# Optimization experiments

Measured on AMD Instinct MI355X. Metric: run time of the kernel, lower is better.

## Reference

```python
import jax, jax.numpy as jnp
import numpy as np

PT, SKIP, CNN_UNITS, RNN_UNITS = 16, 32, 512, 512


def setup_inputs() -> dict:
    key = jax.random.key(0)
    k_x, k_w, k_u = jax.random.split(key, 3)
    B, T, C, H = 128, 512, CNN_UNITS, RNN_UNITS
    # 0.05 scaling keeps the relu GRU recurrence numerically stable
    x = jax.random.normal(k_x, (B, T, C), dtype=jnp.float32)
    W = jax.random.normal(k_w, (C, 3 * H), dtype=jnp.float32) * 0.05
    U = jax.random.normal(k_u, (H, 3 * H), dtype=jnp.float32) * 0.05
    b = jnp.zeros((2, 3 * H), dtype=jnp.float32)  # [input_bias, recurrent_bias] (reset_after=True)
    return {"x": x, "W": W, "U": U, "b": b}


def reference(x, W, U, b):
    B, T, C = x.shape
    H = U.shape[0]
    pt, skip = PT, SKIP
    # pretrans: last pt*skip steps -> (B, pt, skip, C) -> (B, skip, pt, C) -> (B*skip, pt, C)
    s = x[:, -pt * skip:, :]
    s = s.reshape(B, pt, skip, C).transpose(0, 2, 1, 3).reshape(B * skip, pt, C)
    # precompute input projections for all timesteps: (pt, B*skip, 3H)
    xp = jnp.einsum('ntc,ch->tnh', s, W) + b[0]
    b_rec = b[1]

    def step(h, xt):
        rec = h @ U + b_rec                      # (N, 3H)
        xz, xr, xh = jnp.split(xt, 3, axis=-1)
        rz, rr, rh = jnp.split(rec, 3, axis=-1)
        z = jax.nn.sigmoid(xz + rz)
        r = jax.nn.sigmoid(xr + rr)
        hh = jax.nn.relu(xh + r * rh)            # activation='relu'
        h_new = z * h + (1.0 - z) * hh
        return h_new, None

    h0 = jnp.zeros((B * skip, H), dtype=x.dtype)
    h_final, _ = jax.lax.scan(step, h0, xp)
    # posttrans: (B*skip, H) -> (B, skip*H)
    return h_final.reshape(B, skip * H)
```

## Files before the change

kernel.cpp:

```cpp
#include <hip/hip_runtime.h>
#include <cstddef>


typedef unsigned short u16;
typedef __attribute__((ext_vector_type(8))) short short8;
typedef __attribute__((ext_vector_type(8))) u16 u16x8;
typedef __attribute__((ext_vector_type(4))) float floatx4;

#define MFMA16(a, b, c) __builtin_amdgcn_mfma_f32_16x16x32_bf16((a), (b), (c), 0, 0, 0)

__device__ __forceinline__ u16 f32_to_bf16(float f) {
  union { float f; unsigned int u; } c; c.f = f;
  unsigned int u = c.u + 0x7FFFu + ((c.u >> 16) & 1u);
  return (u16)(u >> 16);
}
__device__ __forceinline__ float bf16_to_f32(u16 v) {
  union { unsigned int u; float f; } c; c.u = ((unsigned int)v) << 16;
  return c.f;
}
__device__ __forceinline__ float sigmoidf_(float x) {
  return 1.0f / (1.0f + __expf(-x));
}
__device__ __forceinline__ void gload_lds16(const void* g, void* l) {
  __builtin_amdgcn_global_load_lds(
      (const __attribute__((address_space(1))) unsigned int*)g,
      (__attribute__((address_space(3))) unsigned int*)l, 16, 0, 0);
}

__global__ __launch_bounds__(256)
void pack_x(const float* __restrict__ x, u16* __restrict__ xb) {
  __shared__ u16 sm[64 * 512];
  const int t = blockIdx.x >> 6;
  const int nb = blockIdx.x & 63;
  const int tid = threadIdx.x;
#pragma unroll
  for (int it = 0; it < 16; ++it) {
    int idx = it * 256 + tid;
    int row = idx >> 6, ch = idx & 63;
    int xrow = (nb * 2 + (row >> 5)) * 512 + t * 32 + (row & 31);
    const float* src = x + (size_t)xrow * 512 + ch * 8;
    floatx4 va = *(const floatx4*)src;
    floatx4 vb = *(const floatx4*)(src + 4);
    u16x8 pk;
    pk[0] = f32_to_bf16(va[0]); pk[1] = f32_to_bf16(va[1]);
    pk[2] = f32_to_bf16(va[2]); pk[3] = f32_to_bf16(va[3]);
    pk[4] = f32_to_bf16(vb[0]); pk[5] = f32_to_bf16(vb[1]);
    pk[6] = f32_to_bf16(vb[2]); pk[7] = f32_to_bf16(vb[3]);
    *(u16x8*)&sm[row * 512 + (ch ^ (row & 7)) * 8] = pk;
  }
  __syncthreads();
  u16* dst = xb + (size_t)blockIdx.x * 32768;
#pragma unroll
  for (int it = 0; it < 16; ++it) {
    int idx = it * 256 + tid;
    int row = idx & 63, g = (idx >> 6) & 3, kt = idx >> 8;
    int ch = kt * 4 + g;
    u16x8 vv = *(const u16x8*)&sm[row * 512 + (ch ^ (row & 7)) * 8];
    *(u16x8*)(dst + (size_t)idx * 8) = vv;
  }
}

__global__ void pack_Bt(const float* __restrict__ W, const float* __restrict__ U,
                        u16* __restrict__ Bt) {
  size_t gid = (size_t)blockIdx.x * 256 + threadIdx.x;
  int col = (int)(gid & 63);
  int g   = (int)((gid >> 6) & 3);
  int kt  = (int)((gid >> 8) & 31);
  int cc  = (int)(gid >> 13);
  int c = cc * 64 + col;
  int k0 = kt * 32 + g * 8;
  u16x8 pk;
#pragma unroll
  for (int j = 0; j < 8; ++j) {
    int k = k0 + j;
    float v = (k < 512) ? W[(size_t)k * 1536 + c] : U[(size_t)(k - 512) * 1536 + c];
    pk[j] = f32_to_bf16(v);
  }
  *(u16x8*)(Bt + gid * 8) = pk;
}

__global__ __launch_bounds__(256)
void gru_step(const u16* __restrict__ xb, const u16* __restrict__ Bt,
              const float* __restrict__ bias,
              const u16* __restrict__ h_in, u16* __restrict__ h_out,
              float* __restrict__ out, int t, int first, int last) {
  __shared__ alignas(16) char sm[32768];
  const int tid = threadIdx.x;
  const int idx = blockIdx.x;
  const int nb = ((idx >> 6) << 3) | (idx & 7);
  const int hb = (idx >> 3) & 7;
  const int w = __builtin_amdgcn_readfirstlane(tid >> 6);
  const int lane = tid & 63;
  const int wy = w >> 1, wx = w & 1;
  const int q = lane >> 4, lc = lane & 15;

  const u16* xbB = xb + (size_t)(t * 64 + nb) * 32768;
  const u16* htB = h_in + (size_t)nb * 32768;
  const int cs0 = hb, cs1 = 8 + hb, cs2 = 16 + hb;

  floatx4 acZ[2][2] = {{{0.f,0.f,0.f,0.f},{0.f,0.f,0.f,0.f}},{{0.f,0.f,0.f,0.f},{0.f,0.f,0.f,0.f}}};
  floatx4 acR[2][2] = {{{0.f,0.f,0.f,0.f},{0.f,0.f,0.f,0.f}},{{0.f,0.f,0.f,0.f},{0.f,0.f,0.f,0.f}}};
  floatx4 acX[2][2] = {{{0.f,0.f,0.f,0.f},{0.f,0.f,0.f,0.f}},{{0.f,0.f,0.f,0.f},{0.f,0.f,0.f,0.f}}};
  floatx4 acH[2][2] = {{{0.f,0.f,0.f,0.f},{0.f,0.f,0.f,0.f}},{{0.f,0.f,0.f,0.f},{0.f,0.f,0.f,0.f}}};

  const int ktall = first ? 16 : 32;
  const int wo = w * 1024;

  auto stage = [&](int kt, int bsel) {
    char* lds = sm + bsel * 16384;
    const char* aS = (const char*)((kt < 16) ? (xbB + (size_t)kt * 2048)
                                             : (htB + (size_t)(kt - 16) * 2048));
    gload_lds16(aS + wo + lane * 16, lds + wo);
    gload_lds16((const char*)(Bt + (size_t)(cs0 * 32 + kt) * 2048) + wo + lane * 16,
                lds + 4096 + wo);
    gload_lds16((const char*)(Bt + (size_t)(cs1 * 32 + kt) * 2048) + wo + lane * 16,
                lds + 8192 + wo);
    gload_lds16((const char*)(Bt + (size_t)(cs2 * 32 + kt) * 2048) + wo + lane * 16,
                lds + 12288 + wo);
  };

  auto compute = [&](int bsel, floatx4 (&acT)[2][2]) {
    const char* lds = sm + bsel * 16384;
    short8 a0 = *(const short8*)(lds + (q * 64 + wy * 32 + lc) * 16);
    short8 a1 = *(const short8*)(lds + (q * 64 + wy * 32 + 16 + lc) * 16);
#pragma unroll
    for (int ci = 0; ci < 2; ++ci) {
      int co = (q * 64 + wx * 32 + ci * 16 + lc) * 16;
      short8 bz = *(const short8*)(lds + 4096 + co);
      short8 br = *(const short8*)(lds + 8192 + co);
      short8 bh = *(const short8*)(lds + 12288 + co);
      acZ[0][ci] = MFMA16(a0, bz, acZ[0][ci]);
      acZ[1][ci] = MFMA16(a1, bz, acZ[1][ci]);
      acR[0][ci] = MFMA16(a0, br, acR[0][ci]);
      acR[1][ci] = MFMA16(a1, br, acR[1][ci]);
      acT[0][ci] = MFMA16(a0, bh, acT[0][ci]);
      acT[1][ci] = MFMA16(a1, bh, acT[1][ci]);
    }
  };

  stage(0, 0);
  __syncthreads();
  for (int kt = 0; kt < 16; ++kt) {
    if (kt + 1 < ktall) stage(kt + 1, (kt + 1) & 1);
    compute(kt & 1, acX);
    __syncthreads();
  }
  if (!first) {
    for (int kt = 16; kt < 32; ++kt) {
      if (kt + 1 < 32) stage(kt + 1, (kt + 1) & 1);
      compute(kt & 1, acH);
      __syncthreads();
    }
  }

  const float* b0 = bias;
  const float* b1 = bias + 1536;
  u16* Ct = (u16*)sm;
#pragma unroll
  for (int ci = 0; ci < 2; ++ci) {
    const int hcl = wx * 32 + ci * 16 + lc;
    const int hg = hb * 64 + hcl;
    const float bz = b0[hg] + b1[hg];
    const float br = b0[512 + hg] + b1[512 + hg];
    const float b0h = b0[1024 + hg];
    const float b1h = b1[1024 + hg];
    const int ktg = hg >> 5;
    const int gg = (hg >> 3) & 3;
    const size_t hbase = (((size_t)nb * 16 + ktg) * 4 + gg) * 64;
#pragma unroll
    for (int mi = 0; mi < 2; ++mi) {
#pragma unroll
      for (int reg = 0; reg < 4; ++reg) {
        const int nl = wy * 32 + mi * 16 + q * 4 + reg;
        const int n = nb * 64 + nl;
        float z = sigmoidf_(acZ[mi][ci][reg] + bz);
        float r = sigmoidf_(acR[mi][ci][reg] + br);
        float hh = acX[mi][ci][reg] + b0h + r * (acH[mi][ci][reg] + b1h);
        hh = fmaxf(hh, 0.0f);
        float hp = 0.0f;
        if (!first) hp = bf16_to_f32(h_in[(hbase + nl) * 8 + (hg & 7)]);
        float v = z * hp + (1.0f - z) * hh;
        if (last) out[(size_t)n * 512 + hg] = v;
        else      Ct[nl * 72 + hcl] = f32_to_bf16(v);
      }
    }
  }
  if (!last) {
    __syncthreads();
#pragma unroll
    for (int i = 0; i < 2; ++i) {
      int e = i * 256 + tid;
      int row = e & 63;
      int g = (e >> 6) & 3;
      int ktl = e >> 8;
      u16x8 vv = *(const u16x8*)(Ct + row * 72 + ktl * 32 + g * 8);
      *(u16x8*)(h_out + ((((size_t)nb * 16 + (hb * 2 + ktl)) * 4 + g) * 64 + row) * 8) = vv;
    }
  }
}

extern "C" void kernel_launch(void* const* d_in, const int* in_sizes, int n_in,
                              void* d_out, int out_size, void* d_ws, size_t ws_size,
                              hipStream_t stream) {
  const float* x = (const float*)d_in[0];
  const float* W = (const float*)d_in[1];
  const float* U = (const float*)d_in[2];
  const float* bias = (const float*)d_in[3];
  float* out = (float*)d_out;

  u16* xb = (u16*)d_ws;
  u16* Bt = xb + (size_t)16 * 64 * 32768;
  u16* h0 = Bt + (size_t)1536 * 1024;
  u16* h1 = h0 + (size_t)4096 * 512;

  pack_x<<<1024, 256, 0, stream>>>(x, xb);
  pack_Bt<<<768, 256, 0, stream>>>(W, U, Bt);

  for (int t = 0; t < 16; ++t) {
    const u16* hin = (t & 1) ? h1 : h0;
    u16* hout = (t & 1) ? h0 : h1;
    gru_step<<<512, 256, 0, stream>>>(
        xb, Bt, bias, hin, hout, out, t, (t == 0) ? 1 : 0, (t == 15) ? 1 : 0);
  }
}
```

Before: 522.1 us.

## Deepen GRU step K-loop to 4-stage LDS pipeline with explicit vmcnt waits

Replaces the double-buffered LDS staging in the per-timestep GRU GEMM with a four-buffer ring that keeps three tiles in flight. It uses explicit s_waitcnt vmcnt counts and raw barriers in place of a full __syncthreads after every tile, and raises wave priority around the MFMA compute. The aim is to hide global-to-LDS load latency better. LDS use doubles to 64KB per block, which may cut occupancy. Because the ternary picks the accumulator array by reference, the compute lambda may get harder for the compiler to keep in registers.

```diff
diff --git a/kernel.cpp b/kernel.cpp
--- a/kernel.cpp
+++ b/kernel.cpp
@@ -84,7 +84,7 @@
               const float* __restrict__ bias,
               const u16* __restrict__ h_in, u16* __restrict__ h_out,
               float* __restrict__ out, int t, int first, int last) {
-  __shared__ alignas(16) char sm[32768];
+  __shared__ alignas(16) char sm[65536];
   const int tid = threadIdx.x;
   const int idx = blockIdx.x;
   const int nb = ((idx >> 6) << 3) | (idx & 7);
@@ -139,20 +139,30 @@
   };
 
   stage(0, 0);
+  stage(1, 1);
+  stage(2, 2);
+  int kt = 0;
+  for (; kt < ktall - 2; ++kt) {
+    asm volatile("s_waitcnt vmcnt(8)" ::: "memory");
+    __builtin_amdgcn_s_barrier();
+    if (kt + 3 < ktall) stage(kt + 3, (kt + 3) & 3);
+    __builtin_amdgcn_s_setprio(1);
+    compute(kt & 3, (kt < 16) ? acX : acH);
+    __builtin_amdgcn_s_setprio(0);
+  }
+  asm volatile("s_waitcnt vmcnt(4)" ::: "memory");
+  __builtin_amdgcn_s_barrier();
+  __builtin_amdgcn_s_setprio(1);
+  compute(kt & 3, (kt < 16) ? acX : acH);
+  __builtin_amdgcn_s_setprio(0);
+  ++kt;
+  asm volatile("s_waitcnt vmcnt(0)" ::: "memory");
+  __builtin_amdgcn_s_barrier();
+  __builtin_amdgcn_s_setprio(1);
+  compute(kt & 3, (kt < 16) ? acX : acH);
+  __builtin_amdgcn_s_setprio(0);
+
   __syncthreads();
-  for (int kt = 0; kt < 16; ++kt) {
-    if (kt + 1 < ktall) stage(kt + 1, (kt + 1) & 1);
-    compute(kt & 1, acX);
-    __syncthreads();
-  }
-  if (!first) {
-    for (int kt = 16; kt < 32; ++kt) {
-      if (kt + 1 < 32) stage(kt + 1, (kt + 1) & 1);
-      compute(kt & 1, acH);
-      __syncthreads();
-    }
-  }
-
   const float* b0 = bias;
   const float* b1 = bias + 1536;
   u16* Ct = (u16*)sm;
```

Result: slower. 597.3 us (+14.4%).

## Enlarge GRU step tile to 128 rows with split-K waves and 4-stage pipeline

Applied to the files above, without the earlier changes.

Each gru_step block now covers 128 batch rows instead of 64, using 512 threads, and the grid shrinks from 512 to 256 blocks. Its 8 waves split the K dimension in two, and the halves are summed through LDS before the gate epilogue. Loads use a 4-slot global-to-LDS ring with explicit vmcnt waits, and the MFMA section runs at raised priority. The aim is to reuse the weight tiles across more rows and hide load latency, at the cost of 144KB of dynamic LDS per block, an extra reduction pass, and fewer blocks across the CUs.

```diff
diff --git a/kernel.cpp b/kernel.cpp
--- a/kernel.cpp
+++ b/kernel.cpp
@@ -79,109 +79,195 @@
   *(u16x8*)(Bt + gid * 8) = pk;
 }
 
-__global__ __launch_bounds__(256)
+__global__ __launch_bounds__(512, 2)
 void gru_step(const u16* __restrict__ xb, const u16* __restrict__ Bt,
               const float* __restrict__ bias,
               const u16* __restrict__ h_in, u16* __restrict__ h_out,
               float* __restrict__ out, int t, int first, int last) {
-  __shared__ alignas(16) char sm[32768];
+  extern __shared__ char sm[];
   const int tid = threadIdx.x;
   const int idx = blockIdx.x;
-  const int nb = ((idx >> 6) << 3) | (idx & 7);
-  const int hb = (idx >> 3) & 7;
+  const int nbb = idx & 31;
+  const int hb  = idx >> 5;
   const int w = __builtin_amdgcn_readfirstlane(tid >> 6);
   const int lane = tid & 63;
-  const int wy = w >> 1, wx = w & 1;
+  const int ks = w & 1, wx = (w >> 1) & 1, wy = w >> 2;
   const int q = lane >> 4, lc = lane & 15;
 
-  const u16* xbB = xb + (size_t)(t * 64 + nb) * 32768;
-  const u16* htB = h_in + (size_t)nb * 32768;
-  const int cs0 = hb, cs1 = 8 + hb, cs2 = 16 + hb;
-
-  floatx4 acZ[2][2] = {{{0.f,0.f,0.f,0.f},{0.f,0.f,0.f,0.f}},{{0.f,0.f,0.f,0.f},{0.f,0.f,0.f,0.f}}};
-  floatx4 acR[2][2] = {{{0.f,0.f,0.f,0.f},{0.f,0.f,0.f,0.f}},{{0.f,0.f,0.f,0.f},{0.f,0.f,0.f,0.f}}};
-  floatx4 acX[2][2] = {{{0.f,0.f,0.f,0.f},{0.f,0.f,0.f,0.f}},{{0.f,0.f,0.f,0.f},{0.f,0.f,0.f,0.f}}};
-  floatx4 acH[2][2] = {{{0.f,0.f,0.f,0.f},{0.f,0.f,0.f,0.f}},{{0.f,0.f,0.f,0.f},{0.f,0.f,0.f,0.f}}};
-
-  const int ktall = first ? 16 : 32;
-  const int wo = w * 1024;
-
-  auto stage = [&](int kt, int bsel) {
-    char* lds = sm + bsel * 16384;
-    const char* aS = (const char*)((kt < 16) ? (xbB + (size_t)kt * 2048)
-                                             : (htB + (size_t)(kt - 16) * 2048));
-    gload_lds16(aS + wo + lane * 16, lds + wo);
-    gload_lds16((const char*)(Bt + (size_t)(cs0 * 32 + kt) * 2048) + wo + lane * 16,
-                lds + 4096 + wo);
-    gload_lds16((const char*)(Bt + (size_t)(cs1 * 32 + kt) * 2048) + wo + lane * 16,
-                lds + 8192 + wo);
-    gload_lds16((const char*)(Bt + (size_t)(cs2 * 32 + kt) * 2048) + wo + lane * 16,
-                lds + 12288 + wo);
+  const u16* xbB0 = xb + (size_t)(t * 64 + nbb * 2) * 32768;
+  const u16* htB0 = h_in + (size_t)(nbb * 2) * 32768;
+
+  floatx4 acZ[4][2], acR[4][2], acX[4][2], acH[4][2];
+#pragma unroll
+  for (int f = 0; f < 4; ++f)
+#pragma unroll
+    for (int ci = 0; ci < 2; ++ci) {
+      acZ[f][ci] = (floatx4){0.f, 0.f, 0.f, 0.f};
+      acR[f][ci] = (floatx4){0.f, 0.f, 0.f, 0.f};
+      acX[f][ci] = (floatx4){0.f, 0.f, 0.f, 0.f};
+      acH[f][ci] = (floatx4){0.f, 0.f, 0.f, 0.f};
+    }
+
+  auto stageSS = [&](int ss) {
+#pragma unroll
+    for (int i = 0; i < 5; ++i) {
+      int l = i * 8 + w;
+      int c = (l >= 20) ? 1 : 0;
+      int p = l - c * 20;
+      int kt = ss * 2 + c;
+      char* dst = sm + ((size_t)((kt) & 3) * 20480 + (size_t)p * 1024);
+      const u16* src;
+      if (p < 8) {
+        int ah = p >> 2, g = p & 3;
+        src = (kt < 16) ? (xbB0 + (size_t)ah * 32768 + (size_t)kt * 2048 + (size_t)g * 512)
+                        : (htB0 + (size_t)ah * 32768 + (size_t)(kt - 16) * 2048 + (size_t)g * 512);
+      } else {
+        int gate = (p - 8) >> 2, g = (p - 8) & 3;
+        int cs = gate * 8 + hb;
+        src = Bt + (size_t)(cs * 32 + kt) * 2048 + (size_t)g * 512;
+      }
+      gload_lds16((const char*)src + lane * 16, dst);
+    }
   };
 
-  auto compute = [&](int bsel, floatx4 (&acT)[2][2]) {
-    const char* lds = sm + bsel * 16384;
-    short8 a0 = *(const short8*)(lds + (q * 64 + wy * 32 + lc) * 16);
-    short8 a1 = *(const short8*)(lds + (q * 64 + wy * 32 + 16 + lc) * 16);
+  auto compute = [&](int slot, floatx4 (&acT)[4][2]) {
+    const char* L = sm + (size_t)slot * 20480;
+    const char* Ab = L + wy * 4096 + q * 1024 + lc * 16;
+    short8 a0 = *(const short8*)(Ab);
+    short8 a1 = *(const short8*)(Ab + 256);
+    short8 a2 = *(const short8*)(Ab + 512);
+    short8 a3 = *(const short8*)(Ab + 768);
+    __builtin_amdgcn_s_setprio(1);
 #pragma unroll
     for (int ci = 0; ci < 2; ++ci) {
-      int co = (q * 64 + wx * 32 + ci * 16 + lc) * 16;
-      short8 bz = *(const short8*)(lds + 4096 + co);
-      short8 br = *(const short8*)(lds + 8192 + co);
-      short8 bh = *(const short8*)(lds + 12288 + co);
+      const char* Bb = L + 8192 + q * 1024 + (wx * 32 + ci * 16 + lc) * 16;
+      short8 bz = *(const short8*)(Bb);
+      short8 br = *(const short8*)(Bb + 4096);
+      short8 bh = *(const short8*)(Bb + 8192);
       acZ[0][ci] = MFMA16(a0, bz, acZ[0][ci]);
       acZ[1][ci] = MFMA16(a1, bz, acZ[1][ci]);
+      acZ[2][ci] = MFMA16(a2, bz, acZ[2][ci]);
+      acZ[3][ci] = MFMA16(a3, bz, acZ[3][ci]);
       acR[0][ci] = MFMA16(a0, br, acR[0][ci]);
       acR[1][ci] = MFMA16(a1, br, acR[1][ci]);
+      acR[2][ci] = MFMA16(a2, br, acR[2][ci]);
+      acR[3][ci] = MFMA16(a3, br, acR[3][ci]);
       acT[0][ci] = MFMA16(a0, bh, acT[0][ci]);
       acT[1][ci] = MFMA16(a1, bh, acT[1][ci]);
-    }
+      acT[2][ci] = MFMA16(a2, bh, acT[2][ci]);
+      acT[3][ci] = MFMA16(a3, bh, acT[3][ci]);
+    }
+    __builtin_amdgcn_s_setprio(0);
   };
 
-  stage(0, 0);
-  __syncthreads();
-  for (int kt = 0; kt < 16; ++kt) {
-    if (kt + 1 < ktall) stage(kt + 1, (kt + 1) & 1);
-    compute(kt & 1, acX);
-    __syncthreads();
-  }
-  if (!first) {
-    for (int kt = 16; kt < 32; ++kt) {
-      if (kt + 1 < 32) stage(kt + 1, (kt + 1) & 1);
-      compute(kt & 1, acH);
-      __syncthreads();
-    }
-  }
-
-  const float* b0 = bias;
-  const float* b1 = bias + 1536;
+  stageSS(0);
+  stageSS(1);
+  if (first) {
+    for (int s = 0; s < 8; ++s) {
+      if (s < 7) asm volatile("s_waitcnt vmcnt(5)" ::: "memory");
+      else       asm volatile("s_waitcnt vmcnt(0)" ::: "memory");
+      __builtin_amdgcn_s_barrier();
+      compute((2 * s + ks) & 3, acX);
+      __builtin_amdgcn_s_barrier();
+      if (s < 6) stageSS(s + 2);
+    }
+  } else {
+    for (int s = 0; s < 8; ++s) {
+      asm volatile("s_waitcnt vmcnt(5)" ::: "memory");
+      __builtin_amdgcn_s_barrier();
+      compute((2 * s + ks) & 3, acX);
+      __builtin_amdgcn_s_barrier();
+      stageSS(s + 2);
+    }
+    for (int s = 8; s < 16; ++s) {
+      if (s < 15) asm volatile("s_waitcnt vmcnt(5)" ::: "memory");
+      else        asm volatile("s_waitcnt vmcnt(0)" ::: "memory");
+      __builtin_amdgcn_s_barrier();
+      compute((2 * s + ks) & 3, acH);
+      __builtin_amdgcn_s_barrier();
+      if (s < 14) stageSS(s + 2);
+    }
+  }
+
+  __syncthreads();
+  float* red = (float*)(sm + 81920);
+  float* myred = red + (size_t)(wy * 2 + wx) * 4096 + (size_t)lane * 64;
+  if (ks == 1) {
+#pragma unroll
+    for (int f = 0; f < 4; ++f)
+#pragma unroll
+      for (int ci = 0; ci < 2; ++ci) {
+        int j0 = f * 2 + ci;
+        *(floatx4*)(myred + ((j0 ^ (lane & 15)) * 4)) = acZ[f][ci];
+        *(floatx4*)(myred + (((8 + j0) ^ (lane & 15)) * 4)) = acR[f][ci];
+      }
+  }
+  __syncthreads();
+  if (ks == 0) {
+#pragma unroll
+    for (int f = 0; f < 4; ++f)
+#pragma unroll
+      for (int ci = 0; ci < 2; ++ci) {
+        int j0 = f * 2 + ci;
+        acZ[f][ci] += *(const floatx4*)(myred + ((j0 ^ (lane & 15)) * 4));
+        acR[f][ci] += *(const floatx4*)(myred + (((8 + j0) ^ (lane & 15)) * 4));
+      }
+  }
+  __syncthreads();
+  if (ks == 1) {
+#pragma unroll
+    for (int f = 0; f < 4; ++f)
+#pragma unroll
+      for (int ci = 0; ci < 2; ++ci) {
+        int j0 = f * 2 + ci;
+        *(floatx4*)(myred + ((j0 ^ (lane & 15)) * 4)) = acX[f][ci];
+        *(floatx4*)(myred + (((8 + j0) ^ (lane & 15)) * 4)) = acH[f][ci];
+      }
+  }
+  __syncthreads();
+  if (ks == 0) {
+#pragma unroll
+    for (int f = 0; f < 4; ++f)
+#pragma unroll
+      for (int ci = 0; ci < 2; ++ci) {
+        int j0 = f * 2 + ci;
+        acX[f][ci] += *(const floatx4*)(myred + ((j0 ^ (lane & 15)) * 4));
+        acH[f][ci] += *(const floatx4*)(myred + (((8 + j0) ^ (lane & 15)) * 4));
+      }
+  }
+  __syncthreads();
+
   u16* Ct = (u16*)sm;
-#pragma unroll
-  for (int ci = 0; ci < 2; ++ci) {
-    const int hcl = wx * 32 + ci * 16 + lc;
-    const int hg = hb * 64 + hcl;
-    const float bz = b0[hg] + b1[hg];
-    const float br = b0[512 + hg] + b1[512 + hg];
-    const float b0h = b0[1024 + hg];
-    const float b1h = b1[1024 + hg];
-    const int ktg = hg >> 5;
-    const int gg = (hg >> 3) & 3;
-    const size_t hbase = (((size_t)nb * 16 + ktg) * 4 + gg) * 64;
-#pragma unroll
-    for (int mi = 0; mi < 2; ++mi) {
-#pragma unroll
-      for (int reg = 0; reg < 4; ++reg) {
-        const int nl = wy * 32 + mi * 16 + q * 4 + reg;
-        const int n = nb * 64 + nl;
-        float z = sigmoidf_(acZ[mi][ci][reg] + bz);
-        float r = sigmoidf_(acR[mi][ci][reg] + br);
-        float hh = acX[mi][ci][reg] + b0h + r * (acH[mi][ci][reg] + b1h);
-        hh = fmaxf(hh, 0.0f);
-        float hp = 0.0f;
-        if (!first) hp = bf16_to_f32(h_in[(hbase + nl) * 8 + (hg & 7)]);
-        float v = z * hp + (1.0f - z) * hh;
-        if (last) out[(size_t)n * 512 + hg] = v;
-        else      Ct[nl * 72 + hcl] = f32_to_bf16(v);
+  if (ks == 0) {
+    const float* b0 = bias;
+    const float* b1 = bias + 1536;
+#pragma unroll
+    for (int ci = 0; ci < 2; ++ci) {
+      const int hcl = wx * 32 + ci * 16 + lc;
+      const int hg = hb * 64 + hcl;
+      const float bz = b0[hg] + b1[hg];
+      const float br = b0[512 + hg] + b1[512 + hg];
+      const float b0h = b0[1024 + hg];
+      const float b1h = b1[1024 + hg];
+      const int ktg = hg >> 5;
+      const int gg = (hg >> 3) & 3;
+      const size_t hbase = ((((size_t)(nbb * 2 + wy) * 16 + ktg) * 4 + gg) * 64);
+#pragma unroll
+      for (int f = 0; f < 4; ++f) {
+#pragma unroll
+        for (int reg = 0; reg < 4; ++reg) {
+          const int nl = wy * 64 + f * 16 + q * 4 + reg;
+          const int n = nbb * 128 + nl;
+          float z = sigmoidf_(acZ[f][ci][reg] + bz);
+          float r = sigmoidf_(acR[f][ci][reg] + br);
+          float hh = acX[f][ci][reg] + b0h + r * (acH[f][ci][reg] + b1h);
+          hh = fmaxf(hh, 0.0f);
+          float hp = 0.0f;
+          if (!first) hp = bf16_to_f32(h_in[(hbase + (nl & 63)) * 8 + (hg & 7)]);
+          float v = z * hp + (1.0f - z) * hh;
+          if (last) out[(size_t)n * 512 + hg] = v;
+          else      Ct[nl * 72 + hcl] = f32_to_bf16(v);
+        }
       }
     }
   }
@@ -189,12 +275,13 @@
     __syncthreads();
 #pragma unroll
     for (int i = 0; i < 2; ++i) {
-      int e = i * 256 + tid;
-      int row = e & 63;
-      int g = (e >> 6) & 3;
-      int ktl = e >> 8;
-      u16x8 vv = *(const u16x8*)(Ct + row * 72 + ktl * 32 + g * 8);
-      *(u16x8*)(h_out + ((((size_t)nb * 16 + (hb * 2 + ktl)) * 4 + g) * 64 + row) * 8) = vv;
+      int e = i * 512 + tid;
+      int row = e & 127, gc = e >> 7;
+      u16x8 vv = *(const u16x8*)(Ct + row * 72 + gc * 8);
+      int nb2 = nbb * 2 + (row >> 6);
+      int ktg = hb * 2 + (gc >> 2);
+      int g = gc & 3;
+      *(u16x8*)(h_out + ((((size_t)nb2 * 16 + ktg) * 4 + g) * 64 + (row & 63)) * 8) = vv;
     }
   }
 }
@@ -213,13 +300,20 @@
   u16* h0 = Bt + (size_t)1536 * 1024;
   u16* h1 = h0 + (size_t)4096 * 512;
 
+  static int attr_set = 0;
+  if (!attr_set) {
+    hipFuncSetAttribute((const void*)gru_step,
+                        hipFuncAttributeMaxDynamicSharedMemorySize, 147456);
+    attr_set = 1;
+  }
+
   pack_x<<<1024, 256, 0, stream>>>(x, xb);
   pack_Bt<<<768, 256, 0, stream>>>(W, U, Bt);
 
   for (int t = 0; t < 16; ++t) {
     const u16* hin = (t & 1) ? h1 : h0;
     u16* hout = (t & 1) ? h0 : h1;
-    gru_step<<<512, 256, 0, stream>>>(
+    gru_step<<<256, 512, 147456, stream>>>(
         xb, Bt, bias, hin, hout, out, t, (t == 0) ? 1 : 0, (t == 15) ? 1 : 0);
   }
 }
```

New measurement: 588.0 us. 12.6% more time.
